# Kernel optimization log

Hardware: AMD Instinct MI355X
Metric: run time of the kernel (lower is better)

Reference implementation:

```python
import jax, jax.numpy as jnp
import numpy as np

B, T, C, H, K = 2, 4096, 2048, 32, 64
DM, DD, DA = 32, 64, 96
CHUNK = 128
NC = T // CHUNK
GN_EPS = 1e-5 * 8.0 ** 2  # eps * head_size_divisor**2


def setup_inputs() -> dict:
    key = jax.random.key(0)
    ks = iter(jax.random.split(key, 40))
    def nrm(shape, s=1.0):
        return jax.random.normal(next(ks), shape, dtype=jnp.float32) * s
    def uni(shape, lo, hi):
        return jax.random.uniform(next(ks), shape, dtype=jnp.float32, minval=lo, maxval=hi)
    return {
        "x": nrm((B, T, C)),
        "shift_state_in": nrm((B, C)),
        "wkv_state_in": jnp.zeros((B, H, K, K), dtype=jnp.float32),
        "time_maa_x": uni((1, 1, C), 0.0, 1.0),
        "time_maa_w": uni((1, 1, C), 0.0, 1.0),
        "time_maa_k": uni((1, 1, C), 0.0, 1.0),
        "time_maa_v": uni((1, 1, C), 0.0, 1.0),
        "time_maa_r": uni((1, 1, C), 0.0, 1.0),
        "time_maa_g": uni((1, 1, C), 0.0, 1.0),
        "time_maa_a": uni((1, 1, C), 0.0, 1.0),
        "time_maa_w1": nrm((C, 6 * DM), 0.01),
        "time_maa_w2": uni((6, DM, C), -0.01, 0.01),
        "time_decay": uni((1, 1, C), -6.0, -1.0),
        "time_decay_w1": nrm((C, DD), 0.02),
        "time_decay_w2": uni((DD, C), -0.01, 0.01),
        "time_faaaa": nrm((H, K), 0.1),
        "a0": nrm((1, 1, C), 0.01),
        "a1": nrm((C, DA), 0.02),
        "a2": nrm((DA, C), 0.1 / np.sqrt(DA)),
        "k_k": jnp.full((1, 1, C), 0.85, dtype=jnp.float32),
        "k_a": jnp.ones((1, 1, C), dtype=jnp.float32),
        "W_r": nrm((C, C), 1.0 / np.sqrt(C)),
        "W_k": nrm((C, C), 1.0 / np.sqrt(C)),
        "W_v": nrm((C, C), 1.0 / np.sqrt(C)),
        "W_g": nrm((C, C), 1.0 / np.sqrt(C)),
        "W_o": nrm((C, C), 1.0 / np.sqrt(C)),
        "gn_weight": jnp.ones((C,), dtype=jnp.float32),
        "gn_bias": jnp.zeros((C,), dtype=jnp.float32),
    }


def _wkv_delta(r, k, v, w_neg, u, kk, iclr, state0):
    # r,k,v,w_neg,kk,iclr: [B,T,C]; u: [H,K]; state0: [B,H,K,K]
    def to_chunks(t):  # [B,T,C] -> [NC,B,H,CHUNK,K]
        return t.reshape(B, NC, CHUNK, H, K).transpose(1, 0, 3, 2, 4)
    chunks = tuple(map(to_chunks, (r, k, v, w_neg, kk, iclr)))
    u4 = u.reshape(1, H, 1, K)
    mid = CHUNK // 2
    tri = jnp.tril(jnp.ones((CHUNK, CHUNK), dtype=bool), -1)
    eye = jnp.eye(CHUNK, dtype=jnp.float32)

    def step(state, chunk):
        r_c, k_c, v_c, w_log, kk_c, iclr_c = chunk
        w_cum = jnp.cumsum(w_log, axis=2)                       # [B,H,cs,K]
        w_cs = jnp.pad(w_cum[:, :, :-1, :], ((0, 0), (0, 0), (1, 0), (0, 0)))
        offset = w_cs[:, :, mid:mid + 1, :]
        r_decay = jnp.exp(jnp.clip(w_cs - offset, -30, 30))
        k_inv = jnp.exp(jnp.clip(offset - w_cum, -30, 30))
        A = jnp.einsum('bhtk,bhsk->bhts', r_c * r_decay, k_c * k_inv)
        A = jnp.where(tri, A, 0.0)
        diag = jnp.einsum('bhtk,bhtk->bht', r_c, u4 * k_c)
        A = A + diag[..., None] * eye                           # diag_embed add
        kk_corr = jnp.einsum('bhtk,bhsk->bhts', kk_c * iclr_c, kk_c)
        kk_corr = jnp.where(tri, kk_corr, 0.0)
        A_total = A - jnp.tril(A @ kk_corr)
        w_intra = jnp.exp(jnp.clip(w_cum - w_log, -30, 30))
        y = A_total @ v_c + (r_c * w_intra) @ state             # [B,H,cs,K]
        wsum = jnp.sum(w_log, axis=2, keepdims=True)            # [B,H,1,K]
        ws = jnp.exp(wsum)
        w_inter = jnp.exp(jnp.clip(wsum - w_cum, -30, 30))
        kv = jnp.einsum('bhtk,bhtv->bhkv', k_c * w_inter, v_c)
        ab = jnp.einsum('bhtk,bhtj->bhkj', -kk_c * w_inter, kk_c * iclr_c)
        state = state * ws + state @ ab + kv                    # ws broadcasts on dim -2, as in torch
        return state, y

    state, ys = jax.lax.scan(step, state0.astype(jnp.float32), chunks)
    out = ys.transpose(1, 0, 3, 2, 4).reshape(B, T, C)
    return out, state


def reference(x, shift_state_in, wkv_state_in, time_maa_x, time_maa_w, time_maa_k,
              time_maa_v, time_maa_r, time_maa_g, time_maa_a, time_maa_w1, time_maa_w2,
              time_decay, time_decay_w1, time_decay_w2, time_faaaa, a0, a1, a2,
              k_k, k_a, W_r, W_k, W_v, W_g, W_o, gn_weight, gn_bias):
    dxprev = jnp.concatenate([shift_state_in[:, None, :], x[:, :-1]], axis=1) - x
    xxx = jnp.tanh((x + dxprev * time_maa_x) @ time_maa_w1)     # [B,T,6*DM]
    m = jnp.einsum('btsd,sdc->sbtc', xxx.reshape(B, T, 6, DM), time_maa_w2)
    mw, mk, mv, mr, mg, ma = m
    xw = x + dxprev * (time_maa_w + mw)
    xk = x + dxprev * (time_maa_k + mk)
    xv = x + dxprev * (time_maa_v + mv)
    xr = x + dxprev * (time_maa_r + mr)
    xg = x + dxprev * (time_maa_g + mg)
    xa = x + dxprev * (time_maa_a + ma)
    r = xr @ W_r
    k = xk @ W_k
    v = xv @ W_v
    g = jax.nn.silu(xg @ W_g)
    w = time_decay + jnp.tanh(xw @ time_decay_w1) @ time_decay_w2
    iclr = jax.nn.sigmoid(a0 + (xa @ a1) @ a2)
    kk4 = (k * k_k).reshape(B, T, H, K)
    kk = (kk4 / jnp.maximum(jnp.linalg.norm(kk4, axis=-1, keepdims=True), 1e-12)).reshape(B, T, C)
    k = k * (1.0 + (iclr - 1.0) * k_a)
    y, wkv_state_out = _wkv_delta(r, k, v, -jnp.exp(w), time_faaaa, kk, iclr, wkv_state_in)
    # GroupNorm(H groups) over flattened tokens
    yg = y.reshape(B * T, H, K)
    mean = yg.mean(axis=-1, keepdims=True)
    var = yg.var(axis=-1, keepdims=True)
    yg = (yg - mean) / jnp.sqrt(var + GN_EPS)
    y = (yg.reshape(B * T, C) * gn_weight + gn_bias).reshape(B, T, C)
    out = (y * g) @ W_o
    return out, x[:, -1], wkv_state_out
```

## Files before the change

### kernel.cpp

```cpp
#include <hip/hip_runtime.h>


typedef unsigned short u16;
typedef unsigned int   u32;
typedef __attribute__((ext_vector_type(8))) short s16x8;
typedef __attribute__((ext_vector_type(4))) float f32x4;

#define DEV __device__ __forceinline__

DEV float b2f(u16 v){ return __uint_as_float(((u32)v) << 16); }
DEV u16 f2b(float f){ u32 u = __float_as_uint(f); return (u16)((u + 0x7fffu + ((u >> 16) & 1u)) >> 16); }
DEV float clip30(float x){ return fminf(fmaxf(x, -30.f), 30.f); }
DEV void up8(uint4 v, float* f){
  f[0]=b2f((u16)(v.x&0xffffu)); f[1]=b2f((u16)(v.x>>16));
  f[2]=b2f((u16)(v.y&0xffffu)); f[3]=b2f((u16)(v.y>>16));
  f[4]=b2f((u16)(v.z&0xffffu)); f[5]=b2f((u16)(v.z>>16));
  f[6]=b2f((u16)(v.w&0xffffu)); f[7]=b2f((u16)(v.w>>16));
}
DEV uint4 pk8(const float* f){
  uint4 v;
  v.x = (u32)f2b(f[0]) | ((u32)f2b(f[1])<<16);
  v.y = (u32)f2b(f[2]) | ((u32)f2b(f[3])<<16);
  v.z = (u32)f2b(f[4]) | ((u32)f2b(f[5])<<16);
  v.w = (u32)f2b(f[6]) | ((u32)f2b(f[7])<<16);
  return v;
}
DEV void unp16(uint4 v, u16* o){
  o[0]=(u16)(v.x&0xffffu); o[1]=(u16)(v.x>>16);
  o[2]=(u16)(v.y&0xffffu); o[3]=(u16)(v.y>>16);
  o[4]=(u16)(v.z&0xffffu); o[5]=(u16)(v.z>>16);
  o[6]=(u16)(v.w&0xffffu); o[7]=(u16)(v.w>>16);
}
DEV void gload16(const u16* g, u16* l){
  __builtin_amdgcn_global_load_lds(
      (const __attribute__((address_space(1))) u32*)g,
      (__attribute__((address_space(3))) u32*)l, 16, 0, 0);
}
#define ZF4 ((f32x4){0.f,0.f,0.f,0.f})

__global__ void transpose5_k(const float* __restrict__ w0, const float* __restrict__ w1,
    const float* __restrict__ w2, const float* __restrict__ w3, const float* __restrict__ w4,
    u16* __restrict__ o0, u16* __restrict__ o1, u16* __restrict__ o2,
    u16* __restrict__ o3, u16* __restrict__ o4){
  __shared__ float tile[32][33];
  const float* ins[5] = {w0,w1,w2,w3,w4};
  u16* outs[5] = {o0,o1,o2,o3,o4};
  const float* in = ins[blockIdx.z];
  u16* out = outs[blockIdx.z];
  int c0 = blockIdx.x*32, r0 = blockIdx.y*32;
  int tx = threadIdx.x, ty = threadIdx.y;
  #pragma unroll
  for (int j=0;j<4;j++) tile[ty + j*8][tx] = in[(size_t)(r0 + ty + j*8)*2048 + c0 + tx];
  __syncthreads();
  #pragma unroll
  for (int j=0;j<4;j++) out[(size_t)(c0 + ty + j*8)*2048 + r0 + tx] = f2b(tile[tx][ty + j*8]);
}

__global__ void transpose6_k(
    const float* __restrict__ i0, const float* __restrict__ i1, const float* __restrict__ i2,
    const float* __restrict__ i3, const float* __restrict__ i4, const float* __restrict__ i5,
    u16* __restrict__ o0, u16* __restrict__ o1, u16* __restrict__ o2,
    u16* __restrict__ o3, u16* __restrict__ o4, u16* __restrict__ o5){
  __shared__ float tile[32][33];
  const float* ins[6] = {i0,i1,i2,i3,i4,i5};
  u16* outs[6] = {o0,o1,o2,o3,o4,o5};
  const int Rs[6] = {2048, 192, 2048, 64, 2048, 96};
  const int Cs[6] = {192, 2048, 64, 2048, 96, 2048};
  int z = blockIdx.z;
  int R = Rs[z], C = Cs[z];
  int c0 = blockIdx.x*32, r0 = blockIdx.y*32;
  if (c0 >= C || r0 >= R) return;
  const float* in = ins[z];
  u16* out = outs[z];
  int tx = threadIdx.x, ty = threadIdx.y;
  #pragma unroll
  for (int j=0;j<4;j++) tile[ty + j*8][tx] = in[(size_t)(r0 + ty + j*8)*C + c0 + tx];
  __syncthreads();
  #pragma unroll
  for (int j=0;j<4;j++) out[(size_t)(c0 + ty + j*8)*R + r0 + tx] = f2b(tile[tx][ty + j*8]);
}

__global__ __launch_bounds__(256) void prep_k(const float* __restrict__ x, const float* __restrict__ shift,
    const float* __restrict__ maax, u16* __restrict__ xmx, u16* __restrict__ dxp, float* __restrict__ out_xlast){
  int e8 = (blockIdx.x*256 + threadIdx.x) * 8;
  int row = e8 >> 11, col = e8 & 2047;
  int t = row & 4095, b = row >> 12;
  const float* xp = x + (size_t)row*2048 + col;
  const float* pp = t ? (x + (size_t)(row-1)*2048 + col) : (shift + (size_t)b*2048 + col);
  float xf[8], pf[8], mf[8], of[8], df[8];
  *(float4*)(xf)   = *(const float4*)(xp);
  *(float4*)(xf+4) = *(const float4*)(xp+4);
  *(float4*)(pf)   = *(const float4*)(pp);
  *(float4*)(pf+4) = *(const float4*)(pp+4);
  *(float4*)(mf)   = *(const float4*)(maax + col);
  *(float4*)(mf+4) = *(const float4*)(maax + col + 4);
  #pragma unroll
  for (int j=0;j<8;j++){ df[j] = pf[j]-xf[j]; of[j] = xf[j] + df[j]*mf[j]; }
  *(uint4*)(xmx + (size_t)row*2048 + col) = pk8(of);
  *(uint4*)(dxp + (size_t)row*2048 + col) = pk8(df);
  if (t == 4095){
    *(float4*)(out_xlast + (size_t)b*2048 + col)     = *(const float4*)(xf);
    *(float4*)(out_xlast + (size_t)b*2048 + col + 4) = *(const float4*)(xf+4);
  }
}

enum { EPI_STORE=0, EPI_TANH=1, EPI_SILU=2, EPI_LERP=3, EPI_ICLR=5, EPI_STORE32=6 };

__global__ __launch_bounds__(256) void lerp6_k(
    const u16* __restrict__ xxx, const u16* __restrict__ w2t,
    const float* __restrict__ x, const u16* __restrict__ dxp,
    const float* __restrict__ ma0, const float* __restrict__ ma1, const float* __restrict__ ma2,
    const float* __restrict__ ma3, const float* __restrict__ ma4, const float* __restrict__ ma5,
    u16* __restrict__ o0, u16* __restrict__ o1, u16* __restrict__ o2,
    u16* __restrict__ o3, u16* __restrict__ o4, u16* __restrict__ o5)
{
  __shared__ u16 As[128][40];
  __shared__ u16 Bs[128][40];
  const int tid = threadIdx.x, lane = tid & 63, wid = tid >> 6;
  const int m0 = blockIdx.x*128, n0 = blockIdx.y*128;
  const int wrow = (wid>>1)*64, wcol = (wid&1)*64;
  const int fr = lane&15, kg = lane>>4;
  const int r_c0 = tid>>2, r_seg = tid&3, r_c1 = r_c0+64;
  const float* maap[6] = {ma0,ma1,ma2,ma3,ma4,ma5};
  u16* outs[6] = {o0,o1,o2,o3,o4,o5};

  float xv_[4][4][4], dxv_[4][4][4];
  #pragma unroll
  for (int m=0;m<4;m++)
    #pragma unroll
    for (int n=0;n<4;n++)
      #pragma unroll
      for (int q=0;q<4;q++){
        int row = m0 + wrow + m*16 + kg*4 + q;
        int col = n0 + wcol + n*16 + fr;
        xv_[m][n][q]  = x[(size_t)row*2048 + col];
        dxv_[m][n][q] = b2f(dxp[(size_t)row*2048 + col]);
      }

  #pragma unroll
  for (int s=0;s<6;s++){
    __syncthreads();
    *(uint4*)(&As[r_c0][r_seg*8]) = *(const uint4*)(xxx + (size_t)(m0+r_c0)*192 + s*32 + r_seg*8);
    *(uint4*)(&As[r_c1][r_seg*8]) = *(const uint4*)(xxx + (size_t)(m0+r_c1)*192 + s*32 + r_seg*8);
    *(uint4*)(&Bs[r_c0][r_seg*8]) = *(const uint4*)(w2t + (size_t)(n0+r_c0)*192 + s*32 + r_seg*8);
    *(uint4*)(&Bs[r_c1][r_seg*8]) = *(const uint4*)(w2t + (size_t)(n0+r_c1)*192 + s*32 + r_seg*8);
    __syncthreads();
    s16x8 a[4], bb[4];
    #pragma unroll
    for (int m=0;m<4;m++) a[m] = *(const s16x8*)(&As[wrow + m*16 + fr][kg*8]);
    #pragma unroll
    for (int n=0;n<4;n++) bb[n] = *(const s16x8*)(&Bs[wcol + n*16 + fr][kg*8]);
    f32x4 acc[4][4];
    #pragma unroll
    for (int m=0;m<4;m++)
      #pragma unroll
      for (int n=0;n<4;n++) acc[m][n] = ZF4;
    #pragma unroll
    for (int m=0;m<4;m++)
      #pragma unroll
      for (int n=0;n<4;n++)
        acc[m][n] = __builtin_amdgcn_mfma_f32_16x16x32_bf16(a[m], bb[n], acc[m][n], 0,0,0);
    #pragma unroll
    for (int n=0;n<4;n++){
      int col = n0 + wcol + n*16 + fr;
      float mv = maap[s][col];
      #pragma unroll
      for (int m=0;m<4;m++)
        #pragma unroll
        for (int q=0;q<4;q++){
          int row = m0 + wrow + m*16 + kg*4 + q;
          outs[s][(size_t)row*2048 + col] = f2b(xv_[m][n][q] + dxv_[m][n][q]*(mv + acc[m][n][q]));
        }
    }
  }
}

template<int EPI>
__global__ __launch_bounds__(512, 2) void gemm256_k(
    const u16* __restrict__ A, const u16* __restrict__ Bt,
    u16* __restrict__ Cout, float* __restrict__ Cout32,
    int M, int N, int K)
{
  __shared__ __align__(16) u16 lds[4*16384];
  const int tid = threadIdx.x, lane = tid & 63;
  int bxx = blockIdx.x, byy = blockIdx.y;
  if (gridDim.x == 32 && gridDim.y == 8){
    int bid = byy * 32 + bxx;
    int xcd = bid & 7, idx = bid >> 3;
    bxx = xcd*4 + (idx & 3);
    byy = idx >> 2;
  } else {
    int nwg = gridDim.x * gridDim.y;
    if ((nwg & 7) == 0){
      int bid = byy * gridDim.x + bxx;
      int cpx = nwg >> 3;
      int swz = (bid & 7) * cpx + (bid >> 3);
      bxx = swz % gridDim.x; byy = swz / gridDim.x;
    }
  }
  const int m0 = bxx * 256, n0 = byy * 256;
  const int wid = tid >> 6;
  const int wm = wid >> 2, wn = wid & 3;
  const int fr = lane & 15, kg = lane >> 4;
  const int NT = K >> 5;
  const int chunk0 = __builtin_amdgcn_readfirstlane(wid) * 2;
  const int lr = lane >> 2, lsl = lane & 3;
  const int gswz = (lsl ^ ((lr >> 1) & 3)) << 3;
  const int kswz = (kg ^ ((fr >> 1) & 3)) << 3;

  f32x4 acc[8][4];
  #pragma unroll
  for (int m=0;m<8;m++)
    #pragma unroll
    for (int n=0;n<4;n++) acc[m][n] = ZF4;

  auto STAGE = [&](int t){
    u16* ab = lds + (t & 3) * 16384;
    u16* bb = ab + 8192;
    int gc = (t << 5) + gswz;
    #pragma unroll
    for (int i=0;i<2;i++){
      int c = chunk0 + i;
      int r = c*16 + lr;
      gload16(A  + (size_t)(m0 + r)*K + gc, ab + c*512);
      gload16(Bt + (size_t)(n0 + r)*K + gc, bb + c*512);
    }
  };

  STAGE(0); STAGE(1); STAGE(2);
  for (int t=0; t<NT; ++t){
    if (t+2 < NT)      { asm volatile("s_waitcnt vmcnt(8)" ::: "memory"); }
    else if (t+1 < NT) { asm volatile("s_waitcnt vmcnt(4)" ::: "memory"); }
    else               { asm volatile("s_waitcnt vmcnt(0)" ::: "memory"); }
    __builtin_amdgcn_s_barrier();
    __builtin_amdgcn_sched_barrier(0);
    if (t+3 < NT) STAGE(t+3);
    const u16* ab = lds + (t & 3) * 16384;
    const u16* bb = ab + 8192;
    s16x8 af[8], bf[4];
    #pragma unroll
    for (int m=0;m<8;m++){
      int r = wm*128 + m*16 + fr;
      af[m] = *(const s16x8*)(ab + r*32 + kswz);
    }
    #pragma unroll
    for (int n=0;n<4;n++){
      int r = wn*64 + n*16 + fr;
      bf[n] = *(const s16x8*)(bb + r*32 + kswz);
    }
    __builtin_amdgcn_s_setprio(1);
    #pragma unroll
    for (int m=0;m<8;m++)
      #pragma unroll
      for (int n=0;n<4;n++)
        acc[m][n] = __builtin_amdgcn_mfma_f32_16x16x32_bf16(af[m], bf[n], acc[m][n], 0,0,0);
    __builtin_amdgcn_s_setprio(0);
  }

  #pragma unroll
  for (int n=0;n<4;n++){
    int ccol = n0 + wn*64 + n*16 + fr;
    #pragma unroll
    for (int m=0;m<8;m++){
      #pragma unroll
      for (int q=0;q<4;q++){
        int row = m0 + wm*128 + m*16 + kg*4 + q;
        float v = acc[m][n][q];
        size_t oidx = (size_t)row*N + ccol;
        if constexpr (EPI == EPI_STORE) Cout[oidx] = f2b(v);
        else if constexpr (EPI == EPI_STORE32) Cout32[oidx] = v;
        else if constexpr (EPI == EPI_SILU) Cout[oidx] = f2b(v / (1.f + __expf(-v)));
      }
    }
  }
}

template<int EPI, bool ASYNC, bool SWZ>
__global__ __launch_bounds__(256) void gemm_k(
    const u16* __restrict__ A, int lda,
    const u16* __restrict__ Bt, int ldb,
    u16* __restrict__ Cout, float* __restrict__ Cout32, int ldc,
    int M, int N, int K,
    const float* __restrict__ e_x, const u16* __restrict__ e_dxp, const float* __restrict__ e_vec)
{
  constexpr int LDW = ASYNC ? 32 : 40;
  __shared__ u16 As[128][LDW];
  __shared__ u16 Bs[128][LDW];
  const int tid = threadIdx.x;
  const int lane = tid & 63, wid = tid >> 6;
  int bxx = blockIdx.x, byy = blockIdx.y;
  if constexpr (SWZ){
    int nwg = gridDim.x * gridDim.y;
    if ((nwg & 7) == 0){
      int bid = byy * gridDim.x + bxx;
      int cpx = nwg >> 3;
      int swz = (bid & 7) * cpx + (bid >> 3);
      bxx = swz % gridDim.x; byy = swz / gridDim.x;
    }
  }
  const int m0 = bxx * 128, n0 = byy * 128;
  const int wrow = (wid >> 1) * 64, wcol = (wid & 1) * 64;
  const int fr = lane & 15, kg = lane >> 4;
  const int r_c0 = tid >> 2, r_seg = tid & 3;
  const int r_c1 = r_c0 + 64;

  f32x4 acc[4][4];
  #pragma unroll
  for (int m=0;m<4;m++)
    #pragma unroll
    for (int n=0;n<4;n++) acc[m][n] = ZF4;

  for (int k0 = 0; k0 < K; k0 += 32) {
    __syncthreads();
    if constexpr (ASYNC) {
      const int w4 = __builtin_amdgcn_readfirstlane(wid);
      const int rr = lane >> 2, seg8 = (lane & 3) * 8;
      #pragma unroll
      for (int i=0;i<2;i++){
        int row = w4*32 + i*16 + rr;
        gload16(A  + (size_t)(m0 + row)*lda + k0 + seg8, &As[w4*32 + i*16][0]);
        gload16(Bt + (size_t)(n0 + row)*ldb + k0 + seg8, &Bs[w4*32 + i*16][0]);
      }
    } else {
      uint4 av0 = *(const uint4*)(A + (size_t)(m0 + r_c0)*lda + k0 + r_seg*8);
      uint4 av1 = *(const uint4*)(A + (size_t)(m0 + r_c1)*lda + k0 + r_seg*8);
      *(uint4*)(&As[r_c0][r_seg*8]) = av0;
      *(uint4*)(&As[r_c1][r_seg*8]) = av1;
      uint4 z = make_uint4(0,0,0,0);
      uint4 bv0 = (n0 + r_c0 < N) ? *(const uint4*)(Bt + (size_t)(n0 + r_c0)*ldb + k0 + r_seg*8) : z;
      uint4 bv1 = (n0 + r_c1 < N) ? *(const uint4*)(Bt + (size_t)(n0 + r_c1)*ldb + k0 + r_seg*8) : z;
      *(uint4*)(&Bs[r_c0][r_seg*8]) = bv0;
      *(uint4*)(&Bs[r_c1][r_seg*8]) = bv1;
    }
    __syncthreads();
    s16x8 a[4], bb[4];
    #pragma unroll
    for (int m=0;m<4;m++) a[m] = *(const s16x8*)(&As[wrow + m*16 + fr][kg*8]);
    #pragma unroll
    for (int n=0;n<4;n++) bb[n] = *(const s16x8*)(&Bs[wcol + n*16 + fr][kg*8]);
    #pragma unroll
    for (int m=0;m<4;m++)
      #pragma unroll
      for (int n=0;n<4;n++)
        acc[m][n] = __builtin_amdgcn_mfma_f32_16x16x32_bf16(a[m], bb[n], acc[m][n], 0,0,0);
  }
  #pragma unroll
  for (int n=0;n<4;n++){
    int ccol = n0 + wcol + n*16 + fr;
    if (ccol >= N) continue;
    #pragma unroll
    for (int m=0;m<4;m++){
      #pragma unroll
      for (int q=0;q<4;q++){
        int row = m0 + wrow + m*16 + kg*4 + q;
        float v = acc[m][n][q];
        size_t oidx = (size_t)row*ldc + ccol;
        if constexpr (EPI == EPI_STORE) Cout[oidx] = f2b(v);
        else if constexpr (EPI == EPI_STORE32) Cout32[oidx] = v;
        else if constexpr (EPI == EPI_TANH) Cout[oidx] = f2b(tanhf(v));
        else if constexpr (EPI == EPI_SILU) Cout[oidx] = f2b(v / (1.f + expf(-v)));
        else if constexpr (EPI == EPI_LERP){
          float xv = e_x[(size_t)row*2048 + ccol];
          float dx = b2f(e_dxp[(size_t)row*2048 + ccol]);
          Cout[oidx] = f2b(xv + dx * (e_vec[ccol] + v));
        }
        else if constexpr (EPI == EPI_ICLR) Cout[oidx] = f2b(1.f / (1.f + expf(-(e_vec[ccol] + v))));
      }
    }
  }
}

__global__ __launch_bounds__(256) void thin2_k(
    const u16* __restrict__ A0, const u16* __restrict__ Bt0, u16* __restrict__ C0, int N0,
    const u16* __restrict__ A1, const u16* __restrict__ Bt1, u16* __restrict__ C1, int N1,
    int K)
{
  const u16* A  = blockIdx.z ? A1 : A0;
  const u16* Bt = blockIdx.z ? Bt1 : Bt0;
  u16* Cout     = blockIdx.z ? C1 : C0;
  const int N   = blockIdx.z ? N1 : N0;
  const int ldc = N;
  const bool do_tanh = (blockIdx.z == 0);
  const int m0 = blockIdx.x * 64, n0 = blockIdx.y * 64;
  if (n0 >= N) return;

  __shared__ u16 As[64][72];
  __shared__ u16 Bs[64][72];
  const int tid = threadIdx.x;
  const int lane = tid & 63, wid = tid >> 6;
  const int wrow = (wid >> 1) * 32, wcol = (wid & 1) * 32;
  const int fr = lane & 15, kg = lane >> 4;
  const int r_c = tid >> 2, r_seg = tid & 3;

  f32x4 acc[2][2];
  #pragma unroll
  for (int m=0;m<2;m++)
    #pragma unroll
    for (int n=0;n<2;n++) acc[m][n] = ZF4;

  for (int k0 = 0; k0 < K; k0 += 64) {
    __syncthreads();
    {
      const u16* as = A + (size_t)(m0 + r_c)*K + k0 + r_seg*16;
      *(uint4*)(&As[r_c][r_seg*16])     = *(const uint4*)(as);
      *(uint4*)(&As[r_c][r_seg*16 + 8]) = *(const uint4*)(as + 8);
      uint4 z = make_uint4(0,0,0,0);
      bool ok = (n0 + r_c < N);
      const u16* bs = Bt + (size_t)(n0 + r_c)*K + k0 + r_seg*16;
      *(uint4*)(&Bs[r_c][r_seg*16])     = ok ? *(const uint4*)(bs) : z;
      *(uint4*)(&Bs[r_c][r_seg*16 + 8]) = ok ? *(const uint4*)(bs + 8) : z;
    }
    __syncthreads();
    #pragma unroll
    for (int ks=0; ks<2; ++ks){
      s16x8 a[2], bb[2];
      #pragma unroll
      for (int m=0;m<2;m++) a[m] = *(const s16x8*)(&As[wrow + m*16 + fr][ks*32 + kg*8]);
      #pragma unroll
      for (int n=0;n<2;n++) bb[n] = *(const s16x8*)(&Bs[wcol + n*16 + fr][ks*32 + kg*8]);
      #pragma unroll
      for (int m=0;m<2;m++)
        #pragma unroll
        for (int n=0;n<2;n++)
          acc[m][n] = __builtin_amdgcn_mfma_f32_16x16x32_bf16(a[m], bb[n], acc[m][n], 0,0,0);
    }
  }
  #pragma unroll
  for (int n=0;n<2;n++){
    int ccol = n0 + wcol + n*16 + fr;
    if (ccol >= N) continue;
    #pragma unroll
    for (int m=0;m<2;m++){
      #pragma unroll
      for (int q=0;q<4;q++){
        int row = m0 + wrow + m*16 + kg*4 + q;
        float v = acc[m][n][q];
        Cout[(size_t)row*ldc + ccol] = f2b(do_tanh ? tanhf(v) : v);
      }
    }
  }
}

template<int EPI>
__global__ __launch_bounds__(256) void gemm_thin_k(
    const u16* __restrict__ A, int lda,
    const u16* __restrict__ Bt, int ldb,
    u16* __restrict__ Cout, int ldc, int N, int K)
{
  __shared__ u16 As[64][72];
  __shared__ u16 Bs[64][72];
  const int tid = threadIdx.x;
  const int lane = tid & 63, wid = tid >> 6;
  const int m0 = blockIdx.x * 64, n0 = blockIdx.y * 64;
  const int wrow = (wid >> 1) * 32, wcol = (wid & 1) * 32;
  const int fr = lane & 15, kg = lane >> 4;
  const int r_c = tid >> 2, r_seg = tid & 3;

  f32x4 acc[2][2];
  #pragma unroll
  for (int m=0;m<2;m++)
    #pragma unroll
    for (int n=0;n<2;n++) acc[m][n] = ZF4;

  for (int k0 = 0; k0 < K; k0 += 64) {
    __syncthreads();
    {
      const u16* as = A + (size_t)(m0 + r_c)*lda + k0 + r_seg*16;
      *(uint4*)(&As[r_c][r_seg*16])     = *(const uint4*)(as);
      *(uint4*)(&As[r_c][r_seg*16 + 8]) = *(const uint4*)(as + 8);
      uint4 z = make_uint4(0,0,0,0);
      bool ok = (n0 + r_c < N);
      const u16* bs = Bt + (size_t)(n0 + r_c)*ldb + k0 + r_seg*16;
      *(uint4*)(&Bs[r_c][r_seg*16])     = ok ? *(const uint4*)(bs) : z;
      *(uint4*)(&Bs[r_c][r_seg*16 + 8]) = ok ? *(const uint4*)(bs + 8) : z;
    }
    __syncthreads();
    #pragma unroll
    for (int ks=0; ks<2; ++ks){
      s16x8 a[2], bb[2];
      #pragma unroll
      for (int m=0;m<2;m++) a[m] = *(const s16x8*)(&As[wrow + m*16 + fr][ks*32 + kg*8]);
      #pragma unroll
      for (int n=0;n<2;n++) bb[n] = *(const s16x8*)(&Bs[wcol + n*16 + fr][ks*32 + kg*8]);
      #pragma unroll
      for (int m=0;m<2;m++)
        #pragma unroll
        for (int n=0;n<2;n++)
          acc[m][n] = __builtin_amdgcn_mfma_f32_16x16x32_bf16(a[m], bb[n], acc[m][n], 0,0,0);
    }
  }
  #pragma unroll
  for (int n=0;n<2;n++){
    int ccol = n0 + wcol + n*16 + fr;
    if (ccol >= N) continue;
    #pragma unroll
    for (int m=0;m<2;m++){
      #pragma unroll
      for (int q=0;q<4;q++){
        int row = m0 + wrow + m*16 + kg*4 + q;
        float v = acc[m][n][q];
        size_t oidx = (size_t)row*ldc + ccol;
        if constexpr (EPI == EPI_TANH) Cout[oidx] = f2b(tanhf(v));
        else Cout[oidx] = f2b(v);
      }
    }
  }
}

__global__ __launch_bounds__(512, 1) void wkv1_k(
    const u16* __restrict__ r_g, const u16* __restrict__ kraw_g, const u16* __restrict__ v_g,
    const u16* __restrict__ ic_g,
    const u16* __restrict__ t2_g, const u16* __restrict__ dw2t_g, const float* __restrict__ td_g,
    const float* __restrict__ u_g, const float* __restrict__ kkk_g, const float* __restrict__ kka_g,
    u16* __restrict__ y1_g, u16* __restrict__ rw_g,
    u16* __restrict__ kvab_g, float* __restrict__ wsA_g)
{
  __shared__ __align__(16) char arena[162304];
  float* WL   = (float*)(arena);
  float* WC   = (float*)(arena + 34816);
  u16* Abuf   = (u16*)(arena);
  u16* kkcT   = (u16*)(arena + 34816);
  float* diag_l = (float*)(arena + 68096);
  float* offs_l = diag_l + 128;
  float* wsum_l = offs_l + 64;
  float* u_l    = wsum_l + 64;
  float* kkk_l  = u_l + 64;
  float* kka_l  = kkk_l + 64;
  float* td_l   = kka_l + 64;
  u16* rd_l   = (u16*)(arena + 70144);
  u16* vT_l   = (u16*)(arena + 70144);
  u16* ki_l   = (u16*)(arena + 88576);
  u16* kkwT_l = (u16*)(arena + 88576);
  u16* kwT_l  = (u16*)(arena + 107008);
  u16* ka_l   = (u16*)(arena + 125440);
  u16* kkb_l  = (u16*)(arena + 143872);
  u16* kaT_l  = (u16*)(arena + 143872);

  const int tid = threadIdx.x, lane = tid & 63, wid = tid >> 6;
  const int cb = blockIdx.x;
  const int c = cb >> 6, b = (cb >> 5) & 1, h = cb & 31;
  const size_t base = ((size_t)(b*4096 + c*128)) * 2048 + h*64;
  const int fr = lane & 15, kg = lane >> 4;
  const int tq = tid >> 2, kh = (tid & 3) * 16;

  {
    const u16* t2s = t2_g + (size_t)(b*4096 + c*128 + tq)*64 + kh;
    *(uint4*)(&rd_l[tq*72 + kh])     = *(const uint4*)(t2s);
    *(uint4*)(&rd_l[tq*72 + kh + 8]) = *(const uint4*)(t2s + 8);
    int n = tid >> 3, sg2 = (tid & 7) * 8;
    *(uint4*)(&ki_l[n*72 + sg2]) = *(const uint4*)(dw2t_g + (size_t)(h*64 + n)*64 + sg2);
  }
  if (tid < 64){
    u_l[tid]   = u_g[h*64 + tid];
    kkk_l[tid] = kkk_g[h*64 + tid];
    kka_l[tid] = kka_g[h*64 + tid];
    td_l[tid]  = td_g[h*64 + tid];
  }
  __syncthreads();
  {
    f32x4 accW[4];
    #pragma unroll
    for (int n=0;n<4;n++) accW[n] = ZF4;
    #pragma unroll
    for (int ks=0; ks<2; ++ks){
      s16x8 af = *(const s16x8*)(&rd_l[(wid*16 + fr)*72 + ks*32 + kg*8]);
      #pragma unroll
      for (int n=0;n<4;n++){
        s16x8 bf = *(const s16x8*)(&ki_l[(n*16 + fr)*72 + ks*32 + kg*8]);
        accW[n] = __builtin_amdgcn_mfma_f32_16x16x32_bf16(af, bf, accW[n], 0,0,0);
      }
    }
    #pragma unroll
    for (int n=0;n<4;n++)
      #pragma unroll
      for (int q=0;q<4;q++){
        int t = wid*16 + kg*4 + q;
        int s = n*16 + fr;
        WL[t*65 + s] = -__expf(td_l[s] + accW[n][q]);
      }
  }
  __syncthreads();
  for (int j=0;j<8;j++){
    int k = wid*8 + j;
    float v = WL[lane*65 + k];
    #pragma unroll
    for (int d=1; d<64; d<<=1){ float o = __shfl_up(v, d); if (lane >= d) v += o; }
    WC[lane*65 + k] = v;
    float carry = __shfl(v, 63);
    float v2 = WL[(64+lane)*65 + k];
    #pragma unroll
    for (int d=1; d<64; d<<=1){ float o = __shfl_up(v2, d); if (lane >= d) v2 += o; }
    v2 += carry;
    WC[(64+lane)*65 + k] = v2;
    float tot = __shfl(v2, 63);
    if (lane == 0){ offs_l[k] = carry; wsum_l[k] = tot; wsA_g[(size_t)cb*64 + k] = __expf(tot); }
  }
  __syncthreads();
  {
    const u16* rs  = r_g    + base + (size_t)tq*2048 + kh;
    const u16* ks_ = kraw_g + base + (size_t)tq*2048 + kh;
    const u16* is_ = ic_g   + base + (size_t)tq*2048 + kh;
    float dpart = 0.f;
    #pragma unroll
    for (int j=0;j<2;j++){
      float rf[8], kf[8], icf[8], rdf[8], kif[8], rwf[8];
      up8(*(const uint4*)(rs + j*8), rf);
      up8(*(const uint4*)(ks_ + j*8), kf);
      up8(*(const uint4*)(is_ + j*8), icf);
      #pragma unroll
      for (int e=0;e<8;e++){
        int k = kh + j*8 + e;
        float kadj = kf[e] * (1.f + (icf[e] - 1.f) * kka_l[k]);
        float wl = WL[tq*65+k], wc = WC[tq*65+k];
        float wcs = wc - wl;
        float off = offs_l[k], wsm = wsum_l[k];
        rdf[e] = rf[e] * __expf(clip30(wcs - off));
        kif[e] = kadj  * __expf(clip30(off - wc));
        rwf[e] = rf[e] * __expf(clip30(wcs));
        kwT_l[k*136 + tq] = f2b(kadj * __expf(clip30(wsm - wc)));
        dpart += rf[e] * u_l[k] * kadj;
      }
      *(uint4*)(&rd_l[tq*72 + kh + j*8]) = pk8(rdf);
      *(uint4*)(&ki_l[tq*72 + kh + j*8]) = pk8(kif);
      *(uint4*)(rw_g + base + (size_t)tq*2048 + kh + j*8) = pk8(rwf);
    }
    dpart += __shfl_xor(dpart, 1);
    dpart += __shfl_xor(dpart, 2);
    if ((tid & 3) == 0) diag_l[tq] = dpart;
  }
  __syncthreads();
  {
    const u16* ks_ = kraw_g + base + (size_t)tq*2048 + kh;
    const u16* is_ = ic_g   + base + (size_t)tq*2048 + kh;
    float kf[16], icf[16], kkraw[16];
    #pragma unroll
    for (int j=0;j<2;j++){
      up8(*(const uint4*)(ks_ + j*8), kf + j*8);
      up8(*(const uint4*)(is_ + j*8), icf + j*8);
    }
    float ss = 0.f;
    #pragma unroll
    for (int e=0;e<16;e++){ kkraw[e] = kf[e]*kkk_l[kh+e]; ss += kkraw[e]*kkraw[e]; }
    ss += __shfl_xor(ss, 1);
    ss += __shfl_xor(ss, 2);
    float rn = 1.f / fmaxf(sqrtf(ss), 1e-12f);
    #pragma unroll
    for (int j=0;j<2;j++){
      float kkb8[8], ka8[8];
      #pragma unroll
      for (int e=0;e<8;e++){
        float kkv = kkraw[j*8+e]*rn;
        kkb8[e] = kkv; ka8[e] = kkv*icf[j*8+e];
      }
      *(uint4*)(&kkb_l[tq*72 + kh + j*8]) = pk8(kkb8);
      *(uint4*)(&ka_l [tq*72 + kh + j*8]) = pk8(ka8);
    }
  }
  __syncthreads();
  f32x4 accA[8];
  #pragma unroll
  for (int n=0;n<8;n++) accA[n] = ZF4;
  #pragma unroll
  for (int ks=0; ks<2; ++ks){
    s16x8 af = *(const s16x8*)(&rd_l[(wid*16 + fr)*72 + ks*32 + kg*8]);
    #pragma unroll
    for (int n=0;n<8;n++){
      s16x8 bf = *(const s16x8*)(&ki_l[(n*16 + fr)*72 + ks*32 + kg*8]);
      accA[n] = __builtin_amdgcn_mfma_f32_16x16x32_bf16(af, bf, accA[n], 0,0,0);
    }
  }
  #pragma unroll
  for (int n=0;n<8;n++)
    #pragma unroll
    for (int q=0;q<4;q++){
      int t = wid*16 + kg*4 + q;
      int s = n*16 + fr;
      float v = accA[n][q];
      v = (t > s) ? v : ((t == s) ? diag_l[t] : 0.f);
      accA[n][q] = v;
      Abuf[t*136 + s] = f2b(v);
    }
  __syncthreads();
  {
    #pragma unroll
    for (int j=0;j<2;j++){
      float kkf[8];
      up8(*(const uint4*)(&kkb_l[tq*72 + kh + j*8]), kkf);
      #pragma unroll
      for (int e=0;e<8;e++){
        int k = kh + j*8 + e;
        kkwT_l[k*136 + tq] = f2b(-kkf[e] * __expf(clip30(wsum_l[k] - WC[tq*65+k])));
      }
    }
  }
  __syncthreads();
  {
    f32x4 accC[8];
    #pragma unroll
    for (int n=0;n<8;n++) accC[n] = ZF4;
    #pragma unroll
    for (int ks=0; ks<2; ++ks){
      s16x8 af = *(const s16x8*)(&ka_l[(wid*16 + fr)*72 + ks*32 + kg*8]);
      #pragma unroll
      for (int n=0;n<8;n++){
        s16x8 bf = *(const s16x8*)(&kkb_l[(n*16 + fr)*72 + ks*32 + kg*8]);
        accC[n] = __builtin_amdgcn_mfma_f32_16x16x32_bf16(af, bf, accC[n], 0,0,0);
      }
    }
    #pragma unroll
    for (int n=0;n<8;n++)
      #pragma unroll
      for (int q=0;q<4;q++){
        int t = wid*16 + kg*4 + q;
        int s = n*16 + fr;
        kkcT[s*136 + t] = f2b((t > s) ? accC[n][q] : 0.f);
      }
  }
  __syncthreads();
  {
    const u16* vs = v_g + base + (size_t)tq*2048 + kh;
    #pragma unroll
    for (int j=0;j<2;j++){
      u16 el[8]; unp16(*(const uint4*)(vs + j*8), el);
      #pragma unroll
      for (int e=0;e<8;e++) vT_l[(kh + j*8 + e)*136 + tq] = el[e];
    }
    #pragma unroll
    for (int j=0;j<2;j++){
      u16 el2[8]; unp16(*(const uint4*)(&ka_l[tq*72 + kh + j*8]), el2);
      #pragma unroll
      for (int e=0;e<8;e++) kaT_l[(kh + j*8 + e)*136 + tq] = el2[e];
    }
  }
  {
    f32x4 accP[8];
    #pragma unroll
    for (int n=0;n<8;n++) accP[n] = ZF4;
    #pragma unroll
    for (int ks=0; ks<4; ++ks){
      s16x8 af = *(const s16x8*)(&Abuf[(wid*16 + fr)*136 + ks*32 + kg*8]);
      #pragma unroll
      for (int n=0;n<8;n++){
        s16x8 bf = *(const s16x8*)(&kkcT[(n*16 + fr)*136 + ks*32 + kg*8]);
        accP[n] = __builtin_amdgcn_mfma_f32_16x16x32_bf16(af, bf, accP[n], 0,0,0);
      }
    }
    #pragma unroll
    for (int n=0;n<8;n++)
      #pragma unroll
      for (int q=0;q<4;q++){
        int t = wid*16 + kg*4 + q;
        int s = n*16 + fr;
        float v = accA[n][q] - ((t >= s) ? accP[n][q] : 0.f);
        Abuf[t*136 + s] = f2b(v);
      }
  }
  __syncthreads();
  {
    f32x4 accY[4];
    #pragma unroll
    for (int n=0;n<4;n++) accY[n] = ZF4;
    #pragma unroll
    for (int ks=0; ks<4; ++ks){
      s16x8 af = *(const s16x8*)(&Abuf[(wid*16 + fr)*136 + ks*32 + kg*8]);
      #pragma unroll
      for (int n=0;n<4;n++){
        s16x8 bf = *(const s16x8*)(&vT_l[(n*16 + fr)*136 + ks*32 + kg*8]);
        accY[n] = __builtin_amdgcn_mfma_f32_16x16x32_bf16(af, bf, accY[n], 0,0,0);
      }
    }
    #pragma unroll
    for (int n=0;n<4;n++)
      #pragma unroll
      for (int q=0;q<4;q++){
        int t = wid*16 + kg*4 + q;
        int vd = n*16 + fr;
        y1_g[base + (size_t)t*2048 + vd] = f2b(accY[n][q]);
      }
  }
  {
    const int isAB = wid >> 2, mrow = (wid & 3) * 16;
    const u16* Amat = isAB ? kkwT_l : kwT_l;
    const u16* Bmat = isAB ? kaT_l  : vT_l;
    f32x4 acc2[4];
    #pragma unroll
    for (int n=0;n<4;n++) acc2[n] = ZF4;
    #pragma unroll
    for (int ks=0; ks<4; ++ks){
      s16x8 af = *(const s16x8*)(&Amat[(mrow + fr)*136 + ks*32 + kg*8]);
      #pragma unroll
      for (int n=0;n<4;n++){
        s16x8 bf = *(const s16x8*)(&Bmat[(n*16 + fr)*136 + ks*32 + kg*8]);
        acc2[n] = __builtin_amdgcn_mfma_f32_16x16x32_bf16(af, bf, acc2[n], 0,0,0);
      }
    }
    u16* kvp = kvab_g + (size_t)cb*8192 + isAB*4096;
    #pragma unroll
    for (int n=0;n<4;n++)
      #pragma unroll
      for (int q=0;q<4;q++){
        int kd = mrow + kg*4 + q, vd = n*16 + fr;
        if (isAB) kvp[vd*64 + kd] = f2b(acc2[n][q]);
        else      kvp[kd*64 + vd] = f2b(acc2[n][q]);
      }
  }
}

__global__ __launch_bounds__(256) void wkv2_k(
   const float* __restrict__ state_in, const u16* __restrict__ kvab_g,
   const float* __restrict__ wsA_g, float* __restrict__ sin_g, float* __restrict__ out_state)
{
  __shared__ u16 Sb[16][72];
  __shared__ u16 abT[64][72];
  const int tid = threadIdx.x, lane = tid & 63, wid = tid >> 6;
  const int blk = blockIdx.x;
  const int bh = blk >> 2, rg = blk & 3;
  const int b = bh >> 5, h = bh & 31;
  const int fr = lane & 15, kg = lane >> 4;
  const int lrow = kg*4;
  const int grow = rg*16 + lrow;
  const int vcol = wid*16 + fr;
  const int vrow = tid >> 2, jc = (tid & 3) * 16;

  f32x4 S;
  #pragma unroll
  for (int q=0;q<4;q++)
    S[q] = state_in[(size_t)bh*4096 + (size_t)(grow+q)*64 + vcol];

  uint4 pf_ab0, pf_ab1; u16 pf_kv[4]; float pf_ws;
  {
    int cb = b*32 + h;
    const u16* kvp = kvab_g + (size_t)cb*8192;
    pf_ab0 = *(const uint4*)(kvp + 4096 + vrow*64 + jc);
    pf_ab1 = *(const uint4*)(kvp + 4096 + vrow*64 + jc + 8);
    #pragma unroll
    for (int q=0;q<4;q++) pf_kv[q] = kvp[(grow+q)*64 + vcol];
    pf_ws = wsA_g[(size_t)cb*64 + vcol];
  }

  for (int c=0;c<32;c++){
    int cb = (c*2+b)*32 + h;
    *(uint4*)(&abT[vrow][jc])   = pf_ab0;
    *(uint4*)(&abT[vrow][jc+8]) = pf_ab1;
    #pragma unroll
    for (int q=0;q<4;q++) Sb[lrow+q][vcol] = f2b(S[q]);
    float kvf[4];
    #pragma unroll
    for (int q=0;q<4;q++) kvf[q] = b2f(pf_kv[q]);
    float wsf = pf_ws;
    float* sip = sin_g + (size_t)cb*4096;
    #pragma unroll
    for (int q=0;q<4;q++) sip[(size_t)(grow+q)*64 + vcol] = S[q];
    __syncthreads();
    if (c < 31){
      int cb2 = ((c+1)*2+b)*32 + h;
      const u16* kvp2 = kvab_g + (size_t)cb2*8192;
      pf_ab0 = *(const uint4*)(kvp2 + 4096 + vrow*64 + jc);
      pf_ab1 = *(const uint4*)(kvp2 + 4096 + vrow*64 + jc + 8);
      #pragma unroll
      for (int q=0;q<4;q++) pf_kv[q] = kvp2[(grow+q)*64 + vcol];
      pf_ws = wsA_g[(size_t)cb2*64 + vcol];
    }
    f32x4 acc = ZF4;
    #pragma unroll
    for (int ks=0; ks<2; ++ks){
      s16x8 a  = *(const s16x8*)(&Sb[fr][ks*32 + kg*8]);
      s16x8 bb = *(const s16x8*)(&abT[wid*16 + fr][ks*32 + kg*8]);
      acc = __builtin_amdgcn_mfma_f32_16x16x32_bf16(a, bb, acc, 0,0,0);
    }
    #pragma unroll
    for (int q=0;q<4;q++)
      S[q] = S[q]*wsf + acc[q] + kvf[q];
    __syncthreads();
  }
  #pragma unroll
  for (int q=0;q<4;q++)
    out_state[(size_t)bh*4096 + (size_t)(grow+q)*64 + vcol] = S[q];
}

__global__ __launch_bounds__(256) void wkv3_k(
   const u16* __restrict__ y1_g, const u16* __restrict__ rw_g,
   const float* __restrict__ sin_g,
   const u16* __restrict__ g_g, const float* __restrict__ gnw, const float* __restrict__ gnb,
   u16* __restrict__ yf_g)
{
  __shared__ float S_l[64][65];
  __shared__ u16 rw_l[128][72];
  int tid = threadIdx.x;
  int cb = blockIdx.x; int c = cb>>6, b = (cb>>5)&1, h = cb&31;
  size_t base = ((size_t)(b*4096 + c*128))*2048 + h*64;
  const float* sip = sin_g + (size_t)cb*4096;
  #pragma unroll
  for (int j=0;j<16;j++){ int flat = tid*16+j; S_l[flat>>6][flat&63] = sip[flat]; }
  {
    int t = tid>>1, kh = (tid&1)*32;
    const u16* rs = rw_g + base + (size_t)t*2048 + kh;
    #pragma unroll
    for (int j=0;j<4;j++) *(uint4*)(&rw_l[t][kh+j*8]) = *(const uint4*)(rs + j*8);
  }
  __syncthreads();
  int t = tid>>1, vh = (tid&1)*32;
  float acc[32];
  #pragma unroll
  for (int j=0;j<32;j++) acc[j] = 0.f;
  for (int kf2=0; kf2<64; kf2++){
    float rv = b2f(rw_l[t][kf2]);
    #pragma unroll
    for (int j=0;j<32;j++) acc[j] += rv * S_l[kf2][vh+j];
  }
  float sum=0.f, sq=0.f;
  float yv[32];
  #pragma unroll
  for (int j=0;j<32;j++){
    yv[j] = acc[j] + b2f(y1_g[base + (size_t)t*2048 + vh + j]);
    sum += yv[j]; sq += yv[j]*yv[j];
  }
  sum += __shfl_xor(sum, 1); sq += __shfl_xor(sq, 1);
  float mean = sum * (1.f/64.f);
  float var = sq * (1.f/64.f) - mean*mean;
  float rstd = rsqrtf(fmaxf(var, 0.f) + 6.4e-4f);
  size_t bt = (size_t)(b*4096 + c*128 + t);
  #pragma unroll
  for (int j=0;j<32;j++){
    int ch = h*64 + vh + j;
    float val = (yv[j]-mean)*rstd * gnw[ch] + gnb[ch];
    val *= b2f(g_g[bt*2048 + ch]);
    yf_g[base + (size_t)t*2048 + vh + j] = f2b(val);
  }
}

#define O_WTR   0ull
#define O_WTK   8388608ull
#define O_WTV   16777216ull
#define O_WTG   25165824ull
#define O_WTO   33554432ull
#define O_W1T   41943040ull
#define O_W2T   42729472ull
#define O_DW1T  43515904ull
#define O_DW2T  43778048ull
#define O_A1T   44040192ull
#define O_A2T   44433408ull
#define O_XXX   44826624ull
#define O_T2    47972352ull
#define O_T3    49020928ull
#define O_WSA   50593792ull
#define O_XMX   51118080ull
#define O_A     84672512ull
#define O_I     118226944ull
#define O_R     151781376ull
#define O_K     185335808ull
#define O_V     218890240ull
#define WS_NEEDED 252444672ull

extern "C" void kernel_launch(void* const* d_in, const int* in_sizes, int n_in,
                              void* d_out, int out_size, void* d_ws, size_t ws_size,
                              hipStream_t stream)
{
  (void)in_sizes; (void)n_in; (void)out_size;
  if (ws_size < WS_NEEDED) return;
  const float* x     = (const float*)d_in[0];
  const float* shift = (const float*)d_in[1];
  const float* st_in = (const float*)d_in[2];
  const float* maax  = (const float*)d_in[3];
  const float* maas[6] = {(const float*)d_in[4],(const float*)d_in[5],(const float*)d_in[6],
                          (const float*)d_in[7],(const float*)d_in[8],(const float*)d_in[9]};
  const float* w1    = (const float*)d_in[10];
  const float* w2    = (const float*)d_in[11];
  const float* td    = (const float*)d_in[12];
  const float* dw1   = (const float*)d_in[13];
  const float* dw2   = (const float*)d_in[14];
  const float* faaaa = (const float*)d_in[15];
  const float* a0v   = (const float*)d_in[16];
  const float* a1w   = (const float*)d_in[17];
  const float* a2w   = (const float*)d_in[18];
  const float* kkk   = (const float*)d_in[19];
  const float* kka   = (const float*)d_in[20];
  const float* Wr    = (const float*)d_in[21];
  const float* Wk    = (const float*)d_in[22];
  const float* Wv    = (const float*)d_in[23];
  const float* Wg    = (const float*)d_in[24];
  const float* Wo    = (const float*)d_in[25];
  const float* gnw   = (const float*)d_in[26];
  const float* gnb   = (const float*)d_in[27];
  float* out = (float*)d_out;
  char* ws = (char*)d_ws;
  #define WSP(o) ((u16*)(ws + (o)))

  u16 *wtR=WSP(O_WTR), *wtK=WSP(O_WTK), *wtV=WSP(O_WTV), *wtG=WSP(O_WTG), *wtO=WSP(O_WTO);
  u16 *w1t=WSP(O_W1T), *w2t=WSP(O_W2T), *dw1t=WSP(O_DW1T), *dw2t=WSP(O_DW2T), *a1t=WSP(O_A1T), *a2t=WSP(O_A2T);
  u16 *xxx=WSP(O_XXX), *t2b=WSP(O_T2), *t3b=WSP(O_T3);
  u16 *sXMX=WSP(O_XMX), *sA=WSP(O_A), *sI=WSP(O_I), *sR=WSP(O_R), *sK=WSP(O_K), *sV=WSP(O_V);
  u16 *rw = WSP(O_WTR);
  float* sinF = (float*)(ws + O_XMX);
  float* wsA = (float*)(ws + O_WSA);
  float* out_xlast = out + 16777216;
  float* out_state = out + 16781312;

  dim3 tb(32,8);
  transpose5_k<<<dim3(64,64,5), tb, 0, stream>>>(Wr, Wk, Wv, Wg, Wo, wtR, wtK, wtV, wtG, wtO);
  transpose6_k<<<dim3(64,64,6), tb, 0, stream>>>(w1, w2, dw1, dw2, a1w, a2w,
                                                 w1t, w2t, dw1t, dw2t, a1t, a2t);

  prep_k<<<8192, 256, 0, stream>>>(x, shift, maax, sXMX , sI , out_xlast);

  gemm_thin_k<EPI_TANH><<<dim3(128,3), 256, 0, stream>>>(sXMX, 2048, w1t, 2048, xxx, 192, 192, 2048);
  lerp6_k<<<dim3(64,16), 256, 0, stream>>>(xxx, w2t, x, sI ,
      maas[0], maas[1], maas[2], maas[3], maas[4], maas[5],
      sXMX , sA , sR , sK , sV , sI );
  thin2_k<<<dim3(128,2,2), 256, 0, stream>>>(sXMX, dw1t, t2b, 64, sI, a1t, t3b, 96, 2048);
  gemm_k<EPI_ICLR,true,true><<<dim3(64,16), 256, 0, stream>>>(t3b, 96, a2t, 96, sI, nullptr, 2048, 8192, 2048, 96, nullptr, nullptr, a0v);
  gemm256_k<EPI_STORE><<<dim3(32,8), 512, 0, stream>>>(sK, wtR, sXMX, nullptr, 8192, 2048, 2048);
  gemm256_k<EPI_STORE><<<dim3(32,8), 512, 0, stream>>>(sA, wtK, sK, nullptr, 8192, 2048, 2048);
  gemm256_k<EPI_STORE><<<dim3(32,8), 512, 0, stream>>>(sR, wtV, sA, nullptr, 8192, 2048, 2048);
  gemm256_k<EPI_SILU><<<dim3(32,8), 512, 0, stream>>>(sV, wtG, sR, nullptr, 8192, 2048, 2048);
  wkv1_k<<<2048, 512, 0, stream>>>(sXMX, sK, sA, sI, t2b, dw2t, td, faaaa, kkk, kka,
                                   sK, rw, sV, wsA);
  wkv2_k<<<256, 256, 0, stream>>>(st_in, sV, wsA, sinF, out_state);
  wkv3_k<<<2048, 256, 0, stream>>>(sK, rw, sinF, sR , gnw, gnb, sK );
  gemm256_k<EPI_STORE32><<<dim3(32,8), 512, 0, stream>>>(sK, wtO, nullptr, out, 8192, 2048, 2048);
}
```

Baseline: 938.2 us.

## Shrink big GEMM tiles to 128x128 and merge wkv1 prep phases

The five large projection GEMMs move from 256x256 tiles with 512 threads and a 4-stage LDS ring to 128x128 tiles with 256 threads, a 3-stage ring, and 1024 workgroups. The hard-coded XCD remap for the 32x8 grid is dropped in favour of the generic swizzle. The intent is more workgroups across CUs and better occupancy, at the cost of less operand reuse per tile and a shallower prefetch pipeline. Separately, wkv1 fuses its two per-token prep passes into one. That removes a barrier and repeated global loads of k and iclr, but keeps more values live in registers at once.

```diff
diff --git a/kernel.cpp b/kernel.cpp
--- a/kernel.cpp
+++ b/kernel.cpp
@@ -176,20 +176,15 @@
 }
 
 template<int EPI>
-__global__ __launch_bounds__(512, 2) void gemm256_k(
+__global__ __launch_bounds__(256, 3) void gemm128_k(
     const u16* __restrict__ A, const u16* __restrict__ Bt,
     u16* __restrict__ Cout, float* __restrict__ Cout32,
     int M, int N, int K)
 {
-  __shared__ __align__(16) u16 lds[4*16384];
+  __shared__ __align__(16) u16 lds[3*8192];
   const int tid = threadIdx.x, lane = tid & 63;
   int bxx = blockIdx.x, byy = blockIdx.y;
-  if (gridDim.x == 32 && gridDim.y == 8){
-    int bid = byy * 32 + bxx;
-    int xcd = bid & 7, idx = bid >> 3;
-    bxx = xcd*4 + (idx & 3);
-    byy = idx >> 2;
-  } else {
+  {
     int nwg = gridDim.x * gridDim.y;
     if ((nwg & 7) == 0){
       int bid = byy * gridDim.x + bxx;
@@ -198,9 +193,9 @@
       bxx = swz % gridDim.x; byy = swz / gridDim.x;
     }
   }
-  const int m0 = bxx * 256, n0 = byy * 256;
+  const int m0 = bxx * 128, n0 = byy * 128;
   const int wid = tid >> 6;
-  const int wm = wid >> 2, wn = wid & 3;
+  const int wm = wid >> 1, wn = wid & 1;
   const int fr = lane & 15, kg = lane >> 4;
   const int NT = K >> 5;
   const int chunk0 = __builtin_amdgcn_readfirstlane(wid) * 2;
@@ -208,15 +203,15 @@
   const int gswz = (lsl ^ ((lr >> 1) & 3)) << 3;
   const int kswz = (kg ^ ((fr >> 1) & 3)) << 3;
 
-  f32x4 acc[8][4];
-  #pragma unroll
-  for (int m=0;m<8;m++)
+  f32x4 acc[4][4];
+  #pragma unroll
+  for (int m=0;m<4;m++)
     #pragma unroll
     for (int n=0;n<4;n++) acc[m][n] = ZF4;
 
   auto STAGE = [&](int t){
-    u16* ab = lds + (t & 3) * 16384;
-    u16* bb = ab + 8192;
+    u16* ab = lds + (t % 3) * 8192;
+    u16* bb = ab + 4096;
     int gc = (t << 5) + gswz;
     #pragma unroll
     for (int i=0;i<2;i++){
@@ -227,20 +222,19 @@
     }
   };
 
-  STAGE(0); STAGE(1); STAGE(2);
+  STAGE(0); STAGE(1);
   for (int t=0; t<NT; ++t){
-    if (t+2 < NT)      { asm volatile("s_waitcnt vmcnt(8)" ::: "memory"); }
-    else if (t+1 < NT) { asm volatile("s_waitcnt vmcnt(4)" ::: "memory"); }
-    else               { asm volatile("s_waitcnt vmcnt(0)" ::: "memory"); }
+    if (t+1 < NT) { asm volatile("s_waitcnt vmcnt(4)" ::: "memory"); }
+    else          { asm volatile("s_waitcnt vmcnt(0)" ::: "memory"); }
     __builtin_amdgcn_s_barrier();
     __builtin_amdgcn_sched_barrier(0);
-    if (t+3 < NT) STAGE(t+3);
-    const u16* ab = lds + (t & 3) * 16384;
-    const u16* bb = ab + 8192;
-    s16x8 af[8], bf[4];
-    #pragma unroll
-    for (int m=0;m<8;m++){
-      int r = wm*128 + m*16 + fr;
+    if (t+2 < NT) STAGE(t+2);
+    const u16* ab = lds + (t % 3) * 8192;
+    const u16* bb = ab + 4096;
+    s16x8 af[4], bf[4];
+    #pragma unroll
+    for (int m=0;m<4;m++){
+      int r = wm*64 + m*16 + fr;
       af[m] = *(const s16x8*)(ab + r*32 + kswz);
     }
     #pragma unroll
@@ -250,7 +244,7 @@
     }
     __builtin_amdgcn_s_setprio(1);
     #pragma unroll
-    for (int m=0;m<8;m++)
+    for (int m=0;m<4;m++)
       #pragma unroll
       for (int n=0;n<4;n++)
         acc[m][n] = __builtin_amdgcn_mfma_f32_16x16x32_bf16(af[m], bf[n], acc[m][n], 0,0,0);
@@ -261,10 +255,10 @@
   for (int n=0;n<4;n++){
     int ccol = n0 + wn*64 + n*16 + fr;
     #pragma unroll
-    for (int m=0;m<8;m++){
+    for (int m=0;m<4;m++){
       #pragma unroll
       for (int q=0;q<4;q++){
-        int row = m0 + wm*128 + m*16 + kg*4 + q;
+        int row = m0 + wm*64 + m*16 + kg*4 + q;
         float v = acc[m][n][q];
         size_t oidx = (size_t)row*N + ccol;
         if constexpr (EPI == EPI_STORE) Cout[oidx] = f2b(v);
@@ -597,64 +591,48 @@
   }
   __syncthreads();
   {
+    float rf[16], kf[16], icf[16], kkraw[16];
     const u16* rs  = r_g    + base + (size_t)tq*2048 + kh;
     const u16* ks_ = kraw_g + base + (size_t)tq*2048 + kh;
     const u16* is_ = ic_g   + base + (size_t)tq*2048 + kh;
-    float dpart = 0.f;
-    #pragma unroll
-    for (int j=0;j<2;j++){
-      float rf[8], kf[8], icf[8], rdf[8], kif[8], rwf[8];
-      up8(*(const uint4*)(rs + j*8), rf);
-      up8(*(const uint4*)(ks_ + j*8), kf);
-      up8(*(const uint4*)(is_ + j*8), icf);
-      #pragma unroll
-      for (int e=0;e<8;e++){
-        int k = kh + j*8 + e;
-        float kadj = kf[e] * (1.f + (icf[e] - 1.f) * kka_l[k]);
-        float wl = WL[tq*65+k], wc = WC[tq*65+k];
-        float wcs = wc - wl;
-        float off = offs_l[k], wsm = wsum_l[k];
-        rdf[e] = rf[e] * __expf(clip30(wcs - off));
-        kif[e] = kadj  * __expf(clip30(off - wc));
-        rwf[e] = rf[e] * __expf(clip30(wcs));
-        kwT_l[k*136 + tq] = f2b(kadj * __expf(clip30(wsm - wc)));
-        dpart += rf[e] * u_l[k] * kadj;
-      }
-      *(uint4*)(&rd_l[tq*72 + kh + j*8]) = pk8(rdf);
-      *(uint4*)(&ki_l[tq*72 + kh + j*8]) = pk8(kif);
-      *(uint4*)(rw_g + base + (size_t)tq*2048 + kh + j*8) = pk8(rwf);
-    }
-    dpart += __shfl_xor(dpart, 1);
-    dpart += __shfl_xor(dpart, 2);
-    if ((tid & 3) == 0) diag_l[tq] = dpart;
-  }
-  __syncthreads();
-  {
-    const u16* ks_ = kraw_g + base + (size_t)tq*2048 + kh;
-    const u16* is_ = ic_g   + base + (size_t)tq*2048 + kh;
-    float kf[16], icf[16], kkraw[16];
-    #pragma unroll
-    for (int j=0;j<2;j++){
-      up8(*(const uint4*)(ks_ + j*8), kf + j*8);
-      up8(*(const uint4*)(is_ + j*8), icf + j*8);
-    }
+    up8(*(const uint4*)(rs),     rf);     up8(*(const uint4*)(rs + 8), rf + 8);
+    up8(*(const uint4*)(ks_),    kf);     up8(*(const uint4*)(ks_ + 8), kf + 8);
+    up8(*(const uint4*)(is_),    icf);    up8(*(const uint4*)(is_ + 8), icf + 8);
     float ss = 0.f;
     #pragma unroll
     for (int e=0;e<16;e++){ kkraw[e] = kf[e]*kkk_l[kh+e]; ss += kkraw[e]*kkraw[e]; }
     ss += __shfl_xor(ss, 1);
     ss += __shfl_xor(ss, 2);
     float rn = 1.f / fmaxf(sqrtf(ss), 1e-12f);
+    float dpart = 0.f;
     #pragma unroll
     for (int j=0;j<2;j++){
-      float kkb8[8], ka8[8];
+      float rdf[8], kif[8], rwf[8], kkb8[8], ka8[8];
       #pragma unroll
       for (int e=0;e<8;e++){
-        float kkv = kkraw[j*8+e]*rn;
-        kkb8[e] = kkv; ka8[e] = kkv*icf[j*8+e];
-      }
+        int i = j*8 + e;
+        int k = kh + i;
+        float kadj = kf[i] * (1.f + (icf[i] - 1.f) * kka_l[k]);
+        float wl = WL[tq*65+k], wc = WC[tq*65+k];
+        float wcs = wc - wl;
+        float off = offs_l[k], wsm = wsum_l[k];
+        rdf[e] = rf[i] * __expf(clip30(wcs - off));
+        kif[e] = kadj  * __expf(clip30(off - wc));
+        rwf[e] = rf[i] * __expf(clip30(wcs));
+        kwT_l[k*136 + tq] = f2b(kadj * __expf(clip30(wsm - wc)));
+        dpart += rf[i] * u_l[k] * kadj;
+        float kkv = kkraw[i]*rn;
+        kkb8[e] = kkv; ka8[e] = kkv*icf[i];
+      }
+      *(uint4*)(&rd_l[tq*72 + kh + j*8])  = pk8(rdf);
+      *(uint4*)(&ki_l[tq*72 + kh + j*8])  = pk8(kif);
       *(uint4*)(&kkb_l[tq*72 + kh + j*8]) = pk8(kkb8);
       *(uint4*)(&ka_l [tq*72 + kh + j*8]) = pk8(ka8);
-    }
+      *(uint4*)(rw_g + base + (size_t)tq*2048 + kh + j*8) = pk8(rwf);
+    }
+    dpart += __shfl_xor(dpart, 1);
+    dpart += __shfl_xor(dpart, 2);
+    if ((tid & 3) == 0) diag_l[tq] = dpart;
   }
   __syncthreads();
   f32x4 accA[8];
@@ -1009,13 +987,13 @@
       sXMX , sA , sR , sK , sV , sI );
   thin2_k<<<dim3(128,2,2), 256, 0, stream>>>(sXMX, dw1t, t2b, 64, sI, a1t, t3b, 96, 2048);
   gemm_k<EPI_ICLR,true,true><<<dim3(64,16), 256, 0, stream>>>(t3b, 96, a2t, 96, sI, nullptr, 2048, 8192, 2048, 96, nullptr, nullptr, a0v);
-  gemm256_k<EPI_STORE><<<dim3(32,8), 512, 0, stream>>>(sK, wtR, sXMX, nullptr, 8192, 2048, 2048);
-  gemm256_k<EPI_STORE><<<dim3(32,8), 512, 0, stream>>>(sA, wtK, sK, nullptr, 8192, 2048, 2048);
-  gemm256_k<EPI_STORE><<<dim3(32,8), 512, 0, stream>>>(sR, wtV, sA, nullptr, 8192, 2048, 2048);
-  gemm256_k<EPI_SILU><<<dim3(32,8), 512, 0, stream>>>(sV, wtG, sR, nullptr, 8192, 2048, 2048);
+  gemm128_k<EPI_STORE><<<dim3(64,16), 256, 0, stream>>>(sK, wtR, sXMX, nullptr, 8192, 2048, 2048);
+  gemm128_k<EPI_STORE><<<dim3(64,16), 256, 0, stream>>>(sA, wtK, sK, nullptr, 8192, 2048, 2048);
+  gemm128_k<EPI_STORE><<<dim3(64,16), 256, 0, stream>>>(sR, wtV, sA, nullptr, 8192, 2048, 2048);
+  gemm128_k<EPI_SILU><<<dim3(64,16), 256, 0, stream>>>(sV, wtG, sR, nullptr, 8192, 2048, 2048);
   wkv1_k<<<2048, 512, 0, stream>>>(sXMX, sK, sA, sI, t2b, dw2t, td, faaaa, kkk, kka,
                                    sK, rw, sV, wsA);
   wkv2_k<<<256, 256, 0, stream>>>(st_in, sV, wsA, sinF, out_state);
   wkv3_k<<<2048, 256, 0, stream>>>(sK, rw, sinF, sR , gnw, gnb, sK );
-  gemm256_k<EPI_STORE32><<<dim3(32,8), 512, 0, stream>>>(sK, wtO, nullptr, out, 8192, 2048, 2048);
-}
+  gemm128_k<EPI_STORE32><<<dim3(64,16), 256, 0, stream>>>(sK, wtO, nullptr, out, 8192, 2048, 2048);
+}
```

After: 1.053 ms. +12.2%, slower.
